# Optimization experiments

Measured on AMD Instinct MI355X. Metric: run time of the kernel, lower is better.

The kernel has to match this reference:

```python
import jax, jax.numpy as jnp
import numpy as np

NUM_EXPERTS = 8
TOP_K = 2
DIM = 1024
HIDDEN = 2048
TOKENS = 8192


def setup_inputs() -> dict:
    key = jax.random.key(0)
    k0, k1, k2, k3, k4 = jax.random.split(key, 5)
    x = jax.random.normal(k0, (TOKENS, DIM), dtype=jnp.float32)
    gate_w = jax.random.normal(k1, (NUM_EXPERTS, DIM), dtype=jnp.float32) * 0.02
    # SwiGLU expert weights, stacked over experts
    w1 = jax.random.normal(k2, (NUM_EXPERTS, DIM, HIDDEN), dtype=jnp.float32) * 0.02
    w3 = jax.random.normal(k3, (NUM_EXPERTS, DIM, HIDDEN), dtype=jnp.float32) * 0.02
    w2 = jax.random.normal(k4, (NUM_EXPERTS, HIDDEN, DIM), dtype=jnp.float32) * 0.02
    return {"x": x, "gate_w": gate_w, "w1": w1, "w3": w3, "w2": w2}


def reference(x, gate_w, w1, w3, w2):
    # x: [T, D]; gate_w: [E, D]; w1,w3: [E, D, H]; w2: [E, H, D]
    E = gate_w.shape[0]
    gate_logits = x @ gate_w.T                               # [T, E]
    topk_vals, topk_idx = jax.lax.top_k(gate_logits, TOP_K)  # [T, K]
    topk_w = jax.nn.softmax(topk_vals.astype(jnp.float32), axis=-1).astype(x.dtype)
    # per-token per-expert combine weight: sum_k w[t,k] * [sel[t,k]==e]  -> [T, E]
    combine = jnp.einsum('tk,tke->te', topk_w,
                         jax.nn.one_hot(topk_idx, E, dtype=x.dtype))
    # SwiGLU experts, computed per expert over all tokens then masked-combined
    h = jnp.einsum('td,edh->eth', x, w1)                     # [E, T, H]
    g = jnp.einsum('td,edh->eth', x, w3)                     # [E, T, H]
    y = jnp.einsum('eth,ehd->etd', jax.nn.silu(h) * g, w2)   # [E, T, D]
    return jnp.einsum('te,etd->td', combine, y)              # [T, D]
```

## Files before the change

### kernel.cpp

```cpp
#include <hip/hip_runtime.h>
#include <cstdint>
#include <cstddef>

#define T_TOKENS 8192
#define DIM      1024
#define HID      2048
#define NE       8
#define HCAP     17408

typedef __attribute__((ext_vector_type(8))) short short8;
typedef __attribute__((ext_vector_type(4))) short short4v;
typedef __attribute__((ext_vector_type(4))) float f32x4;

__device__ __forceinline__ unsigned short f2bf(float f) {
  unsigned int u = __builtin_bit_cast(unsigned int, f);
  u += 0x7fffu + ((u >> 16) & 1u);
  return (unsigned short)(u >> 16);
}

__device__ __forceinline__ float bf2f(unsigned short b) {
  unsigned int u = ((unsigned int)b) << 16;
  return __builtin_bit_cast(float, u);
}

__device__ __forceinline__ void gload16(const void* g, void* lds) {
  __builtin_amdgcn_global_load_lds((const __attribute__((address_space(1))) void*)g,
                                   (__attribute__((address_space(3))) void*)lds,
                                   16, 0, 0);
}

#define PREP_GATE0 12288
__device__ __forceinline__ void transcvt_body(
    const float* __restrict__ in, unsigned short* __restrict__ out,
    int K, int N, int bx, int by, int e, float (*tile)[65], int tid) {
  int r  = tid >> 2;
  int c0 = (tid & 3) * 16;
  const float* src = in + ((size_t)e * K + by * 64 + r) * N + bx * 64 + c0;
#pragma unroll
  for (int j = 0; j < 4; j++) {
    float4 v = *(const float4*)(src + j * 4);
    tile[r][c0 + j * 4 + 0] = v.x; tile[r][c0 + j * 4 + 1] = v.y;
    tile[r][c0 + j * 4 + 2] = v.z; tile[r][c0 + j * 4 + 3] = v.w;
  }
  __syncthreads();
  short8 o0, o1;
#pragma unroll
  for (int j = 0; j < 8; j++) o0[j] = (short)f2bf(tile[c0 + j][r]);
#pragma unroll
  for (int j = 0; j < 8; j++) o1[j] = (short)f2bf(tile[c0 + 8 + j][r]);
  unsigned short* dst = out + ((size_t)e * N + bx * 64 + r) * K + by * 64 + c0;
  *(short8*)dst = o0;
  *(short8*)(dst + 8) = o1;
}

__global__ __launch_bounds__(256) void prep_kernel(
    const float* __restrict__ x, const float* __restrict__ gw,
    const float* __restrict__ w1, const float* __restrict__ w3,
    const float* __restrict__ w2,
    unsigned short* __restrict__ W1T, unsigned short* __restrict__ W3T,
    unsigned short* __restrict__ W2T,
    int2* __restrict__ sel, float2* __restrict__ wts,
    unsigned short* __restrict__ xb,
    int* __restrict__ cnt, unsigned short* __restrict__ zbuf) {
  __shared__ float tile[64][65];
  int bid = blockIdx.x, tid = threadIdx.x;

  if (bid < PREP_GATE0) {
    if (bid < 4096) {
      int t = bid;
      transcvt_body(w1, W1T, DIM, HID, t % 32, (t / 32) % 16, t / 512, tile, tid);
    } else if (bid < 8192) {
      int t = bid - 4096;
      transcvt_body(w3, W3T, DIM, HID, t % 32, (t / 32) % 16, t / 512, tile, tid);
    } else {
      int t = bid - 8192;
      transcvt_body(w2, W2T, HID, DIM, t % 16, (t / 16) % 32, t / 512, tile, tid);
    }
    return;
  }

  if (bid == PREP_GATE0) {
    if (tid < 16) cnt[tid] = 0;
    short8 z = {0, 0, 0, 0, 0, 0, 0, 0};
    if (tid * 8 < 1024) *(short8*)(zbuf + tid * 8) = z;
  }

  int wid = tid >> 6, lane = tid & 63;
  int t = (bid - PREP_GATE0) * 4 + wid;
  const float* xr = x + (size_t)t * DIM;
  unsigned short* xo = xb + (size_t)t * DIM;
  double acc[NE];
#pragma unroll
  for (int e = 0; e < NE; e++) acc[e] = 0.0;
#pragma unroll
  for (int p = 0; p < 4; p++) {
    int idx = p * 256 + lane * 4;
    float4 xv = *(const float4*)(xr + idx);
    short4v o;
    o[0] = (short)f2bf(xv.x); o[1] = (short)f2bf(xv.y);
    o[2] = (short)f2bf(xv.z); o[3] = (short)f2bf(xv.w);
    *(short4v*)(xo + idx) = o;
#pragma unroll
    for (int e = 0; e < NE; e++) {
      float4 g = *(const float4*)(gw + e * DIM + idx);
      acc[e] += (double)xv.x * (double)g.x + (double)xv.y * (double)g.y
              + (double)xv.z * (double)g.z + (double)xv.w * (double)g.w;
    }
  }
#pragma unroll
  for (int e = 0; e < NE; e++) {
    double v = acc[e];
#pragma unroll
    for (int off = 32; off > 0; off >>= 1) v += __shfl_xor(v, off);
    acc[e] = v;
  }
  if (lane == 0) {
    float l[NE];
#pragma unroll
    for (int e = 0; e < NE; e++) l[e] = (float)acc[e];
    int i0 = 0; float v0 = l[0];
#pragma unroll
    for (int e = 1; e < NE; e++) if (l[e] > v0) { v0 = l[e]; i0 = e; }
    int i1 = -1; float v1 = -3.4e38f;
#pragma unroll
    for (int e = 0; e < NE; e++) if (e != i0 && l[e] > v1) { v1 = l[e]; i1 = e; }
    float ew = __expf(v1 - v0);
    float w0 = 1.0f / (1.0f + ew);
    float w1v = ew / (1.0f + ew);
    sel[t] = make_int2(i0, i1);
    wts[t] = make_float2(w0, w1v);
  }
}

__global__ void scatter_kernel(const int2* __restrict__ sel, const float2* __restrict__ wts,
                               int* __restrict__ cnt, int* __restrict__ btok,
                               float* __restrict__ bw, int2* __restrict__ pos) {
  __shared__ int hist[NE];
  __shared__ int base[NE];
  int tid = threadIdx.x;
  if (tid < NE) hist[tid] = 0;
  __syncthreads();
  int t = blockIdx.x * 256 + tid;
  int2 s = sel[t]; float2 w = wts[t];
  int p0 = atomicAdd(&hist[s.x], 1);
  int p1 = atomicAdd(&hist[s.y], 1);
  __syncthreads();
  if (tid < NE) base[tid] = atomicAdd(&cnt[tid], hist[tid]);
  __syncthreads();
  int o0 = base[s.x] + p0;
  btok[s.x * T_TOKENS + o0] = t; bw[s.x * T_TOKENS + o0] = w.x;
  int o1 = base[s.y] + p1;
  btok[s.y * T_TOKENS + o1] = t; bw[s.y * T_TOKENS + o1] = w.y;
  pos[t] = make_int2(o0, o1);
}

__global__ __launch_bounds__(256, 2) void gemm1_kernel(
    const unsigned short* __restrict__ xb, const unsigned short* __restrict__ w1t,
    const unsigned short* __restrict__ w3t, const int* __restrict__ cnt,
    const int* __restrict__ btok, const unsigned short* __restrict__ zbuf,
    unsigned short* __restrict__ h) {
  int e = blockIdx.z;
  int cn = cnt[e];
  int pc = (cn + 127) & ~127;
  int mt = blockIdx.y;
  if (mt * 128 >= pc) return;
  int hoff = 0;
#pragma unroll
  for (int i = 0; i < NE; i++) { int pi = (cnt[i] + 127) & ~127; if (i < e) hoff += pi; }
  int nt = blockIdx.x;

  __shared__ short8 At8[1024];
  __shared__ short8 B18[512];
  __shared__ short8 B38[512];

  int tid = threadIdx.x, wid = tid >> 6, lane = tid & 63;
  int m0 = mt * 128;

  int swzcol = ((lane & 7) ^ (lane >> 3)) * 8;

  const unsigned short* asrc[4];
#pragma unroll
  for (int rd = 0; rd < 4; rd++) {
    int row = (rd * 4 + wid) * 8 + (lane >> 3);
    int r = m0 + row;
    asrc[rd] = (r < cn) ? (xb + (size_t)btok[e * T_TOKENS + r] * DIM + swzcol)
                        : (zbuf + swzcol);
  }
  const unsigned short* b1s[2]; const unsigned short* b3s[2];
#pragma unroll
  for (int rd = 0; rd < 2; rd++) {
    int row = (rd * 4 + wid) * 8 + (lane >> 3);
    size_t o = ((size_t)e * HID + nt * 64 + row) * DIM + swzcol;
    b1s[rd] = w1t + o; b3s[rd] = w3t + o;
  }

  f32x4 zero = {0.f, 0.f, 0.f, 0.f};
  f32x4 acc1[4][2], acc3[4][2];
#pragma unroll
  for (int m = 0; m < 4; m++)
#pragma unroll
    for (int n = 0; n < 2; n++) { acc1[m][n] = zero; acc3[m][n] = zero; }

  int wr = wid >> 1, wc = wid & 1;
  const char* At = (const char*)At8;
  const char* B1 = (const char*)B18;
  const char* B3 = (const char*)B38;
  int lxor = (lane & 7) << 4;

  for (int kt = 0; kt < DIM / 64; kt++) {
    int ko = kt * 64;
#pragma unroll
    for (int rd = 0; rd < 4; rd++)
      gload16(asrc[rd] + ko, (char*)At8 + (rd * 4 + wid) * 1024);
#pragma unroll
    for (int rd = 0; rd < 2; rd++) {
      gload16(b1s[rd] + ko, (char*)B18 + (rd * 4 + wid) * 1024);
      gload16(b3s[rd] + ko, (char*)B38 + (rd * 4 + wid) * 1024);
    }
    __syncthreads();
#pragma unroll
    for (int ks = 0; ks < 2; ks++) {
      int cb = (ks * 64 + (lane >> 4) * 16) ^ lxor;
      short8 a[4], f1[2], f3[2];
#pragma unroll
      for (int m = 0; m < 4; m++)
        a[m] = *(const short8*)(At + (wr * 64 + m * 16 + (lane & 15)) * 128 + cb);
#pragma unroll
      for (int n = 0; n < 2; n++) {
        int rb = (wc * 32 + n * 16 + (lane & 15)) * 128 + cb;
        f1[n] = *(const short8*)(B1 + rb);
        f3[n] = *(const short8*)(B3 + rb);
      }
#pragma unroll
      for (int m = 0; m < 4; m++)
#pragma unroll
        for (int n = 0; n < 2; n++) {
          acc1[m][n] = __builtin_amdgcn_mfma_f32_16x16x32_bf16(a[m], f1[n], acc1[m][n], 0, 0, 0);
          acc3[m][n] = __builtin_amdgcn_mfma_f32_16x16x32_bf16(a[m], f3[n], acc3[m][n], 0, 0, 0);
        }
    }
    __syncthreads();
  }

#pragma unroll
  for (int m = 0; m < 4; m++)
#pragma unroll
    for (int n = 0; n < 2; n++) {
#pragma unroll
      for (int j = 0; j < 4; j++) {
        float s1 = acc1[m][n][j], s3 = acc3[m][n][j];
        float hv = s1 / (1.0f + __expf(-s1)) * s3;
        int row = wr * 64 + m * 16 + (lane >> 4) * 4 + j;
        int col = nt * 64 + wc * 32 + n * 16 + (lane & 15);
        h[(size_t)(hoff + m0 + row) * HID + col] = f2bf(hv);
      }
    }
}

__global__ __launch_bounds__(256, 2) void gemm2_kernel(
    const unsigned short* __restrict__ h, const unsigned short* __restrict__ w2t,
    const int* __restrict__ cnt, const float* __restrict__ bw,
    unsigned short* __restrict__ Y) {
  int e = blockIdx.z;
  int cn = cnt[e];
  int pc = (cn + 127) & ~127;
  int mt = blockIdx.y;
  if (mt * 128 >= pc) return;
  int hoff = 0;
#pragma unroll
  for (int i = 0; i < NE; i++) { int pi = (cnt[i] + 127) & ~127; if (i < e) hoff += pi; }
  int nt = blockIdx.x;

  __shared__ short8 At8[1024];
  __shared__ short8 Bt8[1024];

  int tid = threadIdx.x, wid = tid >> 6, lane = tid & 63;
  int m0 = mt * 128;

  int swzcol = ((lane & 7) ^ (lane >> 3)) * 8;

  const unsigned short* as[4]; const unsigned short* bs[4];
#pragma unroll
  for (int rd = 0; rd < 4; rd++) {
    int row = (rd * 4 + wid) * 8 + (lane >> 3);
    as[rd] = h + (size_t)(hoff + m0 + row) * HID + swzcol;
    bs[rd] = w2t + ((size_t)e * DIM + nt * 128 + row) * HID + swzcol;
  }

  f32x4 zero = {0.f, 0.f, 0.f, 0.f};
  f32x4 acc[4][4];
#pragma unroll
  for (int m = 0; m < 4; m++)
#pragma unroll
    for (int n = 0; n < 4; n++) acc[m][n] = zero;

  int wr = wid >> 1, wc = wid & 1;
  const char* At = (const char*)At8;
  const char* Bt = (const char*)Bt8;
  int lxor = (lane & 7) << 4;

  for (int kt = 0; kt < HID / 64; kt++) {
    int ko = kt * 64;
#pragma unroll
    for (int rd = 0; rd < 4; rd++) {
      gload16(as[rd] + ko, (char*)At8 + (rd * 4 + wid) * 1024);
      gload16(bs[rd] + ko, (char*)Bt8 + (rd * 4 + wid) * 1024);
    }
    __syncthreads();
#pragma unroll
    for (int ks = 0; ks < 2; ks++) {
      int cb = (ks * 64 + (lane >> 4) * 16) ^ lxor;
      short8 a[4], b[4];
#pragma unroll
      for (int m = 0; m < 4; m++)
        a[m] = *(const short8*)(At + (wr * 64 + m * 16 + (lane & 15)) * 128 + cb);
#pragma unroll
      for (int n = 0; n < 4; n++)
        b[n] = *(const short8*)(Bt + (wc * 64 + n * 16 + (lane & 15)) * 128 + cb);
#pragma unroll
      for (int m = 0; m < 4; m++)
#pragma unroll
        for (int n = 0; n < 4; n++)
          acc[m][n] = __builtin_amdgcn_mfma_f32_16x16x32_bf16(a[m], b[n], acc[m][n], 0, 0, 0);
    }
    __syncthreads();
  }

#pragma unroll
  for (int m = 0; m < 4; m++)
#pragma unroll
    for (int j = 0; j < 4; j++) {
      int r = m0 + wr * 64 + m * 16 + (lane >> 4) * 4 + j;
      if (r < cn) {
        float w = bw[e * T_TOKENS + r];
        size_t yb = (size_t)(hoff + r) * DIM + nt * 128 + wc * 64 + (lane & 15);
#pragma unroll
        for (int n = 0; n < 4; n++)
          Y[yb + n * 16] = f2bf(w * acc[m][n][j]);
      }
    }
}

__global__ __launch_bounds__(256) void combine_kernel(
    const unsigned short* __restrict__ Y, const int2* __restrict__ sel,
    const int2* __restrict__ pos, const int* __restrict__ cnt,
    float* __restrict__ out) {
  int hoffs[NE + 1];
  hoffs[0] = 0;
#pragma unroll
  for (int i = 0; i < NE; i++) hoffs[i + 1] = hoffs[i] + ((cnt[i] + 127) & ~127);

  int tid = threadIdx.x;
  int t = blockIdx.x * 2 + (tid >> 7);
  int d0 = (tid & 127) * 8;
  int2 s = sel[t];
  int2 p = pos[t];
  size_t g0 = (size_t)(hoffs[s.x] + p.x) * DIM + d0;
  size_t g1 = (size_t)(hoffs[s.y] + p.y) * DIM + d0;
  short8 a = *(const short8*)(Y + g0);
  short8 b = *(const short8*)(Y + g1);
  float* o = out + (size_t)t * DIM + d0;
  f32x4 lo, hi;
#pragma unroll
  for (int j = 0; j < 4; j++) lo[j] = bf2f((unsigned short)a[j]) + bf2f((unsigned short)b[j]);
#pragma unroll
  for (int j = 0; j < 4; j++) hi[j] = bf2f((unsigned short)a[4 + j]) + bf2f((unsigned short)b[4 + j]);
  *(f32x4*)o = lo;
  *(f32x4*)(o + 4) = hi;
}

extern "C" void kernel_launch(void* const* d_in, const int* in_sizes, int n_in,
                              void* d_out, int out_size, void* d_ws, size_t ws_size,
                              hipStream_t stream) {
  const float* x  = (const float*)d_in[0];
  const float* gw = (const float*)d_in[1];
  const float* w1 = (const float*)d_in[2];
  const float* w3 = (const float*)d_in[3];
  const float* w2 = (const float*)d_in[4];
  float* out = (float*)d_out;

  char* ws = (char*)d_ws;
  unsigned short* W1T = (unsigned short*)ws;
  unsigned short* W3T = W1T + (size_t)NE * HID * DIM;
  unsigned short* W2T = W3T + (size_t)NE * HID * DIM;
  unsigned short* XB  = W2T + (size_t)NE * DIM * HID;
  unsigned short* H   = XB + (size_t)T_TOKENS * DIM;
  int*   TOK = (int*)(H + (size_t)HCAP * HID);
  float* BW  = (float*)(TOK + NE * T_TOKENS);
  int*   CNT = (int*)(BW + NE * T_TOKENS);
  unsigned short* ZBUF = (unsigned short*)(CNT + 16);
  int2*   SEL = (int2*)(ZBUF + 1024);
  float2* WTS = (float2*)(SEL + T_TOKENS);
  int2*   POS = (int2*)(WTS + T_TOKENS);
  unsigned short* Y = W1T;

  prep_kernel<<<14336, 256, 0, stream>>>(x, gw, w1, w3, w2, W1T, W3T, W2T,
                                         SEL, WTS, XB, CNT, ZBUF);
  scatter_kernel<<<T_TOKENS / 256, 256, 0, stream>>>(SEL, WTS, CNT, TOK, BW, POS);
  gemm1_kernel<<<dim3(HID / 64, 64, NE), 256, 0, stream>>>(XB, W1T, W3T, CNT, TOK, ZBUF, H);
  gemm2_kernel<<<dim3(DIM / 128, 64, NE), 256, 0, stream>>>(H, W2T, CNT, BW, Y);
  combine_kernel<<<T_TOKENS / 2, 256, 0, stream>>>(Y, SEL, POS, CNT, out);
}
```

Baseline: 337.3 us.

## Split-K the second expert GEMM into two halves summed in combine

The down-projection GEMM now splits its reduction over the hidden dimension into two halves. Each half runs as a separate block and writes its own bf16 partial output buffer, indexed by compact per-expert offsets. The combine kernel reads and adds both partials for each selected expert. This doubles the number of GEMM2 blocks to fill more compute units, at the cost of extra partial-output traffic and an additional bf16 rounding of each partial.

```diff
diff --git a/kernel.cpp b/kernel.cpp
--- a/kernel.cpp
+++ b/kernel.cpp
@@ -7,6 +7,8 @@
 #define HID      2048
 #define NE       8
 #define HCAP     17408
+
+#define YHALF ((size_t)(2 * T_TOKENS) * DIM)
 
 typedef __attribute__((ext_vector_type(8))) short short8;
 typedef __attribute__((ext_vector_type(4))) short short4v;
@@ -266,16 +268,22 @@
   int pc = (cn + 127) & ~127;
   int mt = blockIdx.y;
   if (mt * 128 >= pc) return;
-  int hoff = 0;
-#pragma unroll
-  for (int i = 0; i < NE; i++) { int pi = (cnt[i] + 127) & ~127; if (i < e) hoff += pi; }
-  int nt = blockIdx.x;
+  int hoff = 0, coff = 0;
+#pragma unroll
+  for (int i = 0; i < NE; i++) {
+    int ci = cnt[i];
+    if (i < e) { hoff += (ci + 127) & ~127; coff += ci; }
+  }
+  int nt = blockIdx.x >> 1;
+  int kh = blockIdx.x & 1;
+  unsigned short* Yk = Y + (size_t)kh * YHALF;
 
   __shared__ short8 At8[1024];
   __shared__ short8 Bt8[1024];
 
   int tid = threadIdx.x, wid = tid >> 6, lane = tid & 63;
   int m0 = mt * 128;
+  int k0 = kh * (HID / 2);
 
   int swzcol = ((lane & 7) ^ (lane >> 3)) * 8;
 
@@ -283,8 +291,8 @@
 #pragma unroll
   for (int rd = 0; rd < 4; rd++) {
     int row = (rd * 4 + wid) * 8 + (lane >> 3);
-    as[rd] = h + (size_t)(hoff + m0 + row) * HID + swzcol;
-    bs[rd] = w2t + ((size_t)e * DIM + nt * 128 + row) * HID + swzcol;
+    as[rd] = h + (size_t)(hoff + m0 + row) * HID + k0 + swzcol;
+    bs[rd] = w2t + ((size_t)e * DIM + nt * 128 + row) * HID + k0 + swzcol;
   }
 
   f32x4 zero = {0.f, 0.f, 0.f, 0.f};
@@ -299,7 +307,7 @@
   const char* Bt = (const char*)Bt8;
   int lxor = (lane & 7) << 4;
 
-  for (int kt = 0; kt < HID / 64; kt++) {
+  for (int kt = 0; kt < HID / 128; kt++) {
     int ko = kt * 64;
 #pragma unroll
     for (int rd = 0; rd < 4; rd++) {
@@ -333,10 +341,10 @@
       int r = m0 + wr * 64 + m * 16 + (lane >> 4) * 4 + j;
       if (r < cn) {
         float w = bw[e * T_TOKENS + r];
-        size_t yb = (size_t)(hoff + r) * DIM + nt * 128 + wc * 64 + (lane & 15);
+        size_t yb = (size_t)(coff + r) * DIM + nt * 128 + wc * 64 + (lane & 15);
 #pragma unroll
         for (int n = 0; n < 4; n++)
-          Y[yb + n * 16] = f2bf(w * acc[m][n][j]);
+          Yk[yb + n * 16] = f2bf(w * acc[m][n][j]);
       }
     }
 }
@@ -345,26 +353,34 @@
     const unsigned short* __restrict__ Y, const int2* __restrict__ sel,
     const int2* __restrict__ pos, const int* __restrict__ cnt,
     float* __restrict__ out) {
-  int hoffs[NE + 1];
-  hoffs[0] = 0;
-#pragma unroll
-  for (int i = 0; i < NE; i++) hoffs[i + 1] = hoffs[i] + ((cnt[i] + 127) & ~127);
+  int coffs[NE + 1];
+  coffs[0] = 0;
+#pragma unroll
+  for (int i = 0; i < NE; i++) coffs[i + 1] = coffs[i] + cnt[i];
+
+  const unsigned short* Y1 = Y + YHALF;
 
   int tid = threadIdx.x;
   int t = blockIdx.x * 2 + (tid >> 7);
   int d0 = (tid & 127) * 8;
   int2 s = sel[t];
   int2 p = pos[t];
-  size_t g0 = (size_t)(hoffs[s.x] + p.x) * DIM + d0;
-  size_t g1 = (size_t)(hoffs[s.y] + p.y) * DIM + d0;
-  short8 a = *(const short8*)(Y + g0);
-  short8 b = *(const short8*)(Y + g1);
+  size_t g0 = (size_t)(coffs[s.x] + p.x) * DIM + d0;
+  size_t g1 = (size_t)(coffs[s.y] + p.y) * DIM + d0;
+  short8 a0 = *(const short8*)(Y + g0);
+  short8 a1 = *(const short8*)(Y1 + g0);
+  short8 b0 = *(const short8*)(Y + g1);
+  short8 b1 = *(const short8*)(Y1 + g1);
   float* o = out + (size_t)t * DIM + d0;
   f32x4 lo, hi;
 #pragma unroll
-  for (int j = 0; j < 4; j++) lo[j] = bf2f((unsigned short)a[j]) + bf2f((unsigned short)b[j]);
-#pragma unroll
-  for (int j = 0; j < 4; j++) hi[j] = bf2f((unsigned short)a[4 + j]) + bf2f((unsigned short)b[4 + j]);
+  for (int j = 0; j < 4; j++)
+    lo[j] = bf2f((unsigned short)a0[j]) + bf2f((unsigned short)a1[j])
+          + bf2f((unsigned short)b0[j]) + bf2f((unsigned short)b1[j]);
+#pragma unroll
+  for (int j = 0; j < 4; j++)
+    hi[j] = bf2f((unsigned short)a0[4 + j]) + bf2f((unsigned short)a1[4 + j])
+          + bf2f((unsigned short)b0[4 + j]) + bf2f((unsigned short)b1[4 + j]);
   *(f32x4*)o = lo;
   *(f32x4*)(o + 4) = hi;
 }
@@ -398,6 +414,6 @@
                                          SEL, WTS, XB, CNT, ZBUF);
   scatter_kernel<<<T_TOKENS / 256, 256, 0, stream>>>(SEL, WTS, CNT, TOK, BW, POS);
   gemm1_kernel<<<dim3(HID / 64, 64, NE), 256, 0, stream>>>(XB, W1T, W3T, CNT, TOK, ZBUF, H);
-  gemm2_kernel<<<dim3(DIM / 128, 64, NE), 256, 0, stream>>>(H, W2T, CNT, BW, Y);
+  gemm2_kernel<<<dim3((DIM / 128) * 2, 64, NE), 256, 0, stream>>>(H, W2T, CNT, BW, Y);
   combine_kernel<<<T_TOKENS / 2, 256, 0, stream>>>(Y, SEL, POS, CNT, out);
 }
```

After: 311.2 us. 1.08x faster.
